# Optimization experiments

Hardware: AMD Instinct MI355X
Metric: run time of the kernel (lower is better)

## Reference

```python
import jax, jax.numpy as jnp
import numpy as np

B, T, D, H = 2, 2048, 1024, 16
DK = D // H
NEG = -1e9  # stand-in for -inf; causal mask guarantees >=1 valid key per row


def setup_inputs() -> dict:
    key = jax.random.key(0)
    ks = jax.random.split(key, 9)
    s = 1.0 / np.sqrt(D)
    x = jax.random.normal(ks[0], (B, T, D), dtype=jnp.float32)
    mask = jnp.broadcast_to(jnp.tril(jnp.ones((T, T), dtype=jnp.int32))[None, None], (B, 1, T, T))
    params = {}
    for i, n in enumerate(['q', 'k', 'v', 'o']):
        params['W' + n] = jax.random.normal(ks[1 + 2 * i], (D, D), dtype=jnp.float32) * s
        params['b' + n] = jax.random.normal(ks[2 + 2 * i], (D,), dtype=jnp.float32) * s
    return dict(x=x, mask=mask, **params)


def reference(x, mask, Wq, bq, Wk, bk, Wv, bv, Wo, bo):
    Bx, Tx, Dx = x.shape
    # projections: [B,T,D] -> [B,H,T,DK]
    def split_heads(y):
        return y.reshape(Bx, Tx, H, DK).transpose(0, 2, 1, 3)
    Q = split_heads(x @ Wq + bq)
    K = split_heads(x @ Wk + bk)
    V = split_heads(x @ Wv + bv)
    scores = jnp.einsum('bhqd,bhkd->bhqk', Q, K) / jnp.sqrt(jnp.float32(DK))
    scores = jnp.where(mask == 0, NEG, scores)
    attn = jax.nn.softmax(scores, axis=-1)  # dropout is identity in eval / p=0
    out = jnp.einsum('bhqk,bhkd->bhqd', attn, V)
    out = out.transpose(0, 2, 1, 3).reshape(Bx, Tx, Dx)
    return out @ Wo + bo
```

## Files before the change

kernel.cpp:

```cpp
#include <hip/hip_runtime.h>
#include <hip/hip_bf16.h>

typedef __bf16 bf16;
typedef __attribute__((ext_vector_type(8))) __bf16 bf16x8;
typedef __attribute__((ext_vector_type(4))) __bf16 bf16x4;
typedef __attribute__((ext_vector_type(4))) float f32x4;

#define TSEQ 2048
#define DMODEL 1024
#define NHEAD 16
#define DKH 64
#define BATCH 2
#define NQKV 3072
#define PSTR 72

typedef __attribute__((address_space(1))) const void gv_t;
typedef __attribute__((address_space(3))) void sv_t;
__device__ __forceinline__ void gll16(const bf16* g, bf16* s) {
    __builtin_amdgcn_global_load_lds((gv_t*)g, (sv_t*)s, 16, 0, 0);
}
__device__ __forceinline__ void wait_vm0() {
    __builtin_amdgcn_s_waitcnt(0x0F70);
}

__global__ __launch_bounds__(256) void prologue(
    const float* __restrict__ x,
    const float* __restrict__ W0, const float* __restrict__ W1,
    const float* __restrict__ W2, const float* __restrict__ W3,
    const float* __restrict__ bq, const float* __restrict__ bk,
    const float* __restrict__ bv,
    bf16* __restrict__ xb, bf16* __restrict__ WT, float* __restrict__ wsBias)
{
    __shared__ float t[32][33];
    const int bid = blockIdx.x, tid = threadIdx.x;
    if (bid < 4096) {
        const int mz = bid >> 10, tt = bid & 1023;
        const float* W = mz == 0 ? W0 : mz == 1 ? W1 : mz == 2 ? W2 : W3;
        bf16* T = WT + (size_t)mz * DMODEL * DMODEL;
        const int bx = (tt & 31) * 32, by = (tt >> 5) * 32;
        const int tx = tid & 31, ty = tid >> 5;
#pragma unroll
        for (int i = 0; i < 4; ++i)
            t[ty + i * 8][tx] = W[(size_t)(by + ty + i * 8) * DMODEL + bx + tx];
        __syncthreads();
#pragma unroll
        for (int i = 0; i < 4; ++i)
            T[(size_t)(bx + ty + i * 8) * DMODEL + by + tx] = (bf16)t[tx][ty + i * 8];
    } else if (bid < 8192) {
        int i = ((bid - 4096) * 256 + tid) * 4;
        f32x4 v = *(const f32x4*)(x + i);
        bf16x4 o;
#pragma unroll
        for (int j = 0; j < 4; ++j) o[j] = (bf16)v[j];
        *(bf16x4*)(xb + i) = o;
    } else {
        int i = (bid - 8192) * 256 + tid;
        wsBias[i] = i < 1024 ? bq[i] : i < 2048 ? bk[i - 1024] : bv[i - 2048];
    }
}

template <typename OutT>
__global__ __launch_bounds__(256) void gemm_bias_kernel(
    const bf16* __restrict__ A, const bf16* __restrict__ BT,
    const float* __restrict__ bias, OutT* __restrict__ C0,
    OutT* __restrict__ C1, int ldc, bf16* __restrict__ Vout, int ksteps)
{
    __shared__ bf16 As[128 * 32];
    __shared__ bf16 Bs[128 * 32];
    const int tid = threadIdx.x;
    const int ln = tid & 63, wave = tid >> 6;
    const int wm = wave >> 1, wn = wave & 1;
    const int lr = ln & 15, quad = ln >> 4;
    const int m0 = blockIdx.y * 128, n0 = blockIdx.x * 128;
    const int k0 = blockIdx.z * ksteps * 32;
    OutT* C = blockIdx.z == 0 ? C0 : C1;

    f32x4 acc[4][4] = {};

    const int grow = wave * 32 + (ln >> 2);
    const int gch = (ln & 3) ^ ((ln >> 2) & 3);
    const bf16* Ag = A + (size_t)(m0 + grow) * DMODEL + gch * 8;
    const bf16* Bg = BT + (size_t)(n0 + grow) * DMODEL + gch * 8;
    bf16* AsW = As + wave * 1024;
    bf16* BsW = Bs + wave * 1024;
    const int rsw = (lr & 3);

    for (int kt = 0; kt < ksteps; ++kt) {
        const int kk = k0 + kt * 32;
        gll16(Ag + kk, AsW);
        gll16(Ag + (size_t)16 * DMODEL + kk, AsW + 512);
        gll16(Bg + kk, BsW);
        gll16(Bg + (size_t)16 * DMODEL + kk, BsW + 512);
        wait_vm0();
        __syncthreads();
        bf16x8 af[4], bfr[4];
#pragma unroll
        for (int i = 0; i < 4; ++i)
            af[i] = *(const bf16x8*)(As + (wm * 64 + i * 16 + lr) * 32 +
                                     ((quad ^ rsw) * 8));
#pragma unroll
        for (int j = 0; j < 4; ++j)
            bfr[j] = *(const bf16x8*)(Bs + (wn * 64 + j * 16 + lr) * 32 +
                                      ((quad ^ rsw) * 8));
#pragma unroll
        for (int i = 0; i < 4; ++i)
#pragma unroll
            for (int j = 0; j < 4; ++j)
                acc[i][j] = __builtin_amdgcn_mfma_f32_16x16x32_bf16(
                    af[i], bfr[j], acc[i][j], 0, 0, 0);
        __syncthreads();
    }

    if (Vout != nullptr && n0 >= 2048) {
        const int bb = m0 >> 11;
        const int tb_ = (m0 & (TSEQ - 1)) + wm * 64;
#pragma unroll
        for (int j = 0; j < 4; ++j) {
            int n = n0 + wn * 64 + j * 16 + lr;
            int hd = n - 2048;
            float bv = bias[n];
            bf16* vrow = Vout + ((size_t)(bb * DMODEL + hd)) * TSEQ;
#pragma unroll
            for (int i = 0; i < 4; ++i) {
                int t = tb_ + i * 16 + quad * 4;
                bf16x4 v4;
#pragma unroll
                for (int r = 0; r < 4; ++r) v4[r] = (bf16)(acc[i][j][r] + bv);
                *(bf16x4*)(vrow + t) = v4;
            }
        }
    } else {
#pragma unroll
        for (int j = 0; j < 4; ++j) {
            int n = n0 + wn * 64 + j * 16 + lr;
            float bv = bias ? bias[n] : 0.f;
#pragma unroll
            for (int i = 0; i < 4; ++i) {
                int mb = m0 + wm * 64 + i * 16 + quad * 4;
#pragma unroll
                for (int r = 0; r < 4; ++r)
                    C[(size_t)(mb + r) * ldc + n] = (OutT)(acc[i][j][r] + bv);
            }
        }
    }
}

__global__ __launch_bounds__(256) void reduce_out(
    const float* __restrict__ P1, const float* __restrict__ bias,
    float* __restrict__ out)
{
    int i = (blockIdx.x * 256 + threadIdx.x) * 4;
    f32x4 a = *(const f32x4*)(out + i);
    f32x4 b = *(const f32x4*)(P1 + i);
    f32x4 bi = *(const f32x4*)(bias + (i & (DMODEL - 1)));
    f32x4 r = a + b + bi;
    *(f32x4*)(out + i) = r;
}

template <bool MASK>
__device__ __forceinline__ void attn_chunk(
    int kc, int q0w, int lr, int quad,
    const bf16* __restrict__ KsB, const bf16* __restrict__ VsB,
    bf16* __restrict__ Pw,
    const bf16x8 qb[2], f32x4 oacc[4], float& lrow)
{
    const int sw = lr & 7;
    bf16x8 kb[4][2];
#pragma unroll
    for (int kt = 0; kt < 4; ++kt)
#pragma unroll
        for (int kk = 0; kk < 2; ++kk)
            kb[kt][kk] = *(const bf16x8*)(KsB + (kt * 16 + lr) * 64 +
                                          (((kk * 4 + quad) ^ sw) * 8));
    f32x4 st[4] = {};
#pragma unroll
    for (int kt = 0; kt < 4; ++kt)
#pragma unroll
        for (int kk = 0; kk < 2; ++kk)
            st[kt] = __builtin_amdgcn_mfma_f32_16x16x32_bf16(
                kb[kt][kk], qb[kk], st[kt], 0, 0, 0);

    const float scale2 = 0.18033688f;
    const int q = q0w + lr;
    float rs = 0.f;
#pragma unroll
    for (int kt = 0; kt < 4; ++kt) {
        bf16x4 p4;
#pragma unroll
        for (int r = 0; r < 4; ++r) {
            float p = exp2f(fmaf(st[kt][r], scale2, -24.0f));
            if (MASK && (kc + kt * 16 + quad * 4 + r > q)) p = 0.f;
            rs += p;
            p4[r] = (bf16)p;
        }
        *(bf16x4*)(Pw + lr * PSTR + kt * 16 + quad * 4) = p4;
    }
    rs += __shfl_xor(rs, 16);
    rs += __shfl_xor(rs, 32);
    lrow += rs;

#pragma unroll
    for (int kk = 0; kk < 2; ++kk) {
        bf16x8 pa = *(const bf16x8*)(Pw + lr * PSTR + kk * 32 + quad * 8);
#pragma unroll
        for (int dt = 0; dt < 4; ++dt) {
            bf16x8 vb = *(const bf16x8*)(VsB + (dt * 16 + lr) * 64 +
                                         (((kk * 4 + quad) ^ sw) * 8));
            oacc[dt] = __builtin_amdgcn_mfma_f32_16x16x32_bf16(
                pa, vb, oacc[dt], 0, 0, 0);
        }
    }
}

__global__ __launch_bounds__(512) void flash_attn(
    const bf16* __restrict__ QKV, const bf16* __restrict__ VT,
    bf16* __restrict__ O)
{
    __shared__ bf16 Ks[2][64 * 64];
    __shared__ bf16 Vs[2][64 * 64];
    __shared__ bf16 Pl[8][16 * PSTR];
    const int tid = threadIdx.x;
    const int ln = tid & 63, w = tid >> 6;
    const int lr = ln & 15, quad = ln >> 4;
    const int h = blockIdx.y, b = blockIdx.z;

    int xb = blockIdx.x;
    if ((h ^ b) & 1) xb = (TSEQ / 128 - 1) - xb;
    const int q0 = xb * 128;
    const int q0w = q0 + w * 16;
    bf16* Pw = Pl[w];

    const bf16* Qb = QKV + (size_t)b * TSEQ * NQKV + h * DKH;
    const bf16* Kb = Qb + 1024;
    const bf16* VTb = VT + (size_t)(b * NHEAD + h) * DKH * TSEQ;

    const int srow = (w & 3) * 16 + (ln >> 3);
    const int scol = ((ln & 7) ^ ((ln >> 3) & 7)) * 8;
    const bool stK = (w < 4);

    auto stage = [&](int buf, int kc) {
        if (stK) {
            const bf16* g = Kb + (size_t)(kc + srow) * NQKV + scol;
            bf16* s = &Ks[buf][(w & 3) * 16 * 64];
#pragma unroll
            for (int l = 0; l < 2; ++l)
                gll16(g + (size_t)(l * 8) * NQKV, s + l * 8 * 64);
        } else {
            const bf16* g = VTb + (size_t)srow * TSEQ + kc + scol;
            bf16* s = &Vs[buf][(w & 3) * 16 * 64];
#pragma unroll
            for (int l = 0; l < 2; ++l)
                gll16(g + (size_t)(l * 8) * TSEQ, s + l * 8 * 64);
        }
    };

    bf16x8 qb[2];
#pragma unroll
    for (int kk = 0; kk < 2; ++kk)
        qb[kk] = *(const bf16x8*)(Qb + (size_t)(q0w + lr) * NQKV +
                                  kk * 32 + quad * 8);

    f32x4 oacc[4] = {};
    float lrow = 0.f;

    const int nch = (q0 + 128) >> 6;
    stage(0, 0);
    wait_vm0();
    __syncthreads();
    for (int c = 0; c < nch; ++c) {
        if (c + 1 < nch) stage((c + 1) & 1, (c + 1) * 64);
        const int kc = c * 64;
        if (kc <= q0w + 15) {
            if (kc + 63 <= q0w)
                attn_chunk<false>(kc, q0w, lr, quad, Ks[c & 1], Vs[c & 1], Pw,
                                  qb, oacc, lrow);
            else
                attn_chunk<true>(kc, q0w, lr, quad, Ks[c & 1], Vs[c & 1], Pw,
                                 qb, oacc, lrow);
        }
        wait_vm0();
        __syncthreads();
    }

#pragma unroll
    for (int r = 0; r < 4; ++r) {
        float inv = 1.0f / __shfl(lrow, quad * 4 + r);
        int row = q0w + quad * 4 + r;
#pragma unroll
        for (int dt = 0; dt < 4; ++dt)
            O[(size_t)(b * TSEQ + row) * DMODEL + h * DKH + dt * 16 + lr] =
                (bf16)(oacc[dt][r] * inv);
    }
}

extern "C" void kernel_launch(void* const* d_in, const int* in_sizes, int n_in,
                              void* d_out, int out_size, void* d_ws, size_t ws_size,
                              hipStream_t stream)
{
    const float* x  = (const float*)d_in[0];
    const float* Wq = (const float*)d_in[2];
    const float* bq = (const float*)d_in[3];
    const float* Wk = (const float*)d_in[4];
    const float* bk = (const float*)d_in[5];
    const float* Wv = (const float*)d_in[6];
    const float* bv = (const float*)d_in[7];
    const float* Wo = (const float*)d_in[8];
    const float* bo = (const float*)d_in[9];

    char* ws = (char*)d_ws;
    bf16* xb   = (bf16*)(ws);
    bf16* QKV  = (bf16*)(ws + (8u  << 20));
    bf16* VT   = (bf16*)(ws + (32u << 20));
    bf16* O    = (bf16*)(ws + (40u << 20));
    bf16* WT   = (bf16*)(ws + (48u << 20));
    float* wsBias = (float*)O;
    float* P1  = (float*)QKV;

    prologue<<<8204, 256, 0, stream>>>(x, Wq, Wk, Wv, Wo, bq, bk, bv,
                                       xb, WT, wsBias);

    gemm_bias_kernel<bf16><<<dim3(NQKV / 128, 32, 1), 256, 0, stream>>>(
        xb, WT, wsBias, QKV, QKV, NQKV, VT, DMODEL / 32);

    flash_attn<<<dim3(TSEQ / 128, NHEAD, BATCH), 512, 0, stream>>>(QKV, VT, O);

    gemm_bias_kernel<float><<<dim3(DMODEL / 128, 32, 2), 256, 0, stream>>>(
        O, WT + 3u * (1u << 20), nullptr, (float*)d_out, P1, DMODEL, nullptr,
        DMODEL / 64);

    reduce_out<<<(BATCH * TSEQ * DMODEL) / 1024, 256, 0, stream>>>(
        P1, bo, (float*)d_out);
}
```

Measured before the change: 232.9 us.

## Multi-stage async LDS pipeline in GEMM and drop split-K output reduction

The GEMM kernel now uses a 4-buffer LDS ring fed by global_load_lds. Three k-steps are prefetched ahead, and partial vmcnt waits replace a full drain plus two barriers per step. The output projection no longer uses a 2-way split-K, so the separate reduce_out kernel and its fp32 partial buffer are removed and the bias is added in the GEMM epilogue. The LDS XOR swizzle is also dropped, which may add bank conflicts. The 64KB of shared memory reduces occupancy, and the output GEMM now runs only 256 blocks.

```diff
diff --git a/kernel.cpp b/kernel.cpp
--- a/kernel.cpp
+++ b/kernel.cpp
@@ -19,8 +19,9 @@
 __device__ __forceinline__ void gll16(const bf16* g, bf16* s) {
     __builtin_amdgcn_global_load_lds((gv_t*)g, (sv_t*)s, 16, 0, 0);
 }
-__device__ __forceinline__ void wait_vm0() {
-    __builtin_amdgcn_s_waitcnt(0x0F70);
+template <int N>
+__device__ __forceinline__ void wait_vm() {
+    __builtin_amdgcn_s_waitcnt(0x0F70 | N);
 }
 
 __global__ __launch_bounds__(256) void prologue(
@@ -62,54 +63,61 @@
 template <typename OutT>
 __global__ __launch_bounds__(256) void gemm_bias_kernel(
     const bf16* __restrict__ A, const bf16* __restrict__ BT,
-    const float* __restrict__ bias, OutT* __restrict__ C0,
-    OutT* __restrict__ C1, int ldc, bf16* __restrict__ Vout, int ksteps)
-{
-    __shared__ bf16 As[128 * 32];
-    __shared__ bf16 Bs[128 * 32];
+    const float* __restrict__ bias, OutT* __restrict__ C, int ldc,
+    bf16* __restrict__ Vout)
+{
+    __shared__ bf16 As[4][128 * 32];
+    __shared__ bf16 Bs[4][128 * 32];
     const int tid = threadIdx.x;
     const int ln = tid & 63, wave = tid >> 6;
     const int wm = wave >> 1, wn = wave & 1;
     const int lr = ln & 15, quad = ln >> 4;
     const int m0 = blockIdx.y * 128, n0 = blockIdx.x * 128;
-    const int k0 = blockIdx.z * ksteps * 32;
-    OutT* C = blockIdx.z == 0 ? C0 : C1;
 
     f32x4 acc[4][4] = {};
 
     const int grow = wave * 32 + (ln >> 2);
-    const int gch = (ln & 3) ^ ((ln >> 2) & 3);
-    const bf16* Ag = A + (size_t)(m0 + grow) * DMODEL + gch * 8;
-    const bf16* Bg = BT + (size_t)(n0 + grow) * DMODEL + gch * 8;
-    bf16* AsW = As + wave * 1024;
-    bf16* BsW = Bs + wave * 1024;
-    const int rsw = (lr & 3);
-
-    for (int kt = 0; kt < ksteps; ++kt) {
-        const int kk = k0 + kt * 32;
-        gll16(Ag + kk, AsW);
-        gll16(Ag + (size_t)16 * DMODEL + kk, AsW + 512);
-        gll16(Bg + kk, BsW);
-        gll16(Bg + (size_t)16 * DMODEL + kk, BsW + 512);
-        wait_vm0();
-        __syncthreads();
+    const int gcol = (ln & 3) * 8;
+    const bf16* Ag = A + (size_t)(m0 + grow) * DMODEL + gcol;
+    const bf16* Bg = BT + (size_t)(n0 + grow) * DMODEL + gcol;
+
+    auto stage = [&](int buf, int kt) {
+        const int kk = kt * 32;
+        bf16* aw = &As[buf][wave * 1024];
+        bf16* bw = &Bs[buf][wave * 1024];
+        gll16(Ag + kk, aw);
+        gll16(Ag + (size_t)16 * DMODEL + kk, aw + 512);
+        gll16(Bg + kk, bw);
+        gll16(Bg + (size_t)16 * DMODEL + kk, bw + 512);
+    };
+
+    auto compute = [&](int buf) {
         bf16x8 af[4], bfr[4];
 #pragma unroll
         for (int i = 0; i < 4; ++i)
-            af[i] = *(const bf16x8*)(As + (wm * 64 + i * 16 + lr) * 32 +
-                                     ((quad ^ rsw) * 8));
+            af[i] = *(const bf16x8*)(&As[buf][(wm * 64 + i * 16 + lr) * 32 + quad * 8]);
 #pragma unroll
         for (int j = 0; j < 4; ++j)
-            bfr[j] = *(const bf16x8*)(Bs + (wn * 64 + j * 16 + lr) * 32 +
-                                      ((quad ^ rsw) * 8));
+            bfr[j] = *(const bf16x8*)(&Bs[buf][(wn * 64 + j * 16 + lr) * 32 + quad * 8]);
 #pragma unroll
         for (int i = 0; i < 4; ++i)
 #pragma unroll
             for (int j = 0; j < 4; ++j)
                 acc[i][j] = __builtin_amdgcn_mfma_f32_16x16x32_bf16(
                     af[i], bfr[j], acc[i][j], 0, 0, 0);
+    };
+
+    stage(0, 0); stage(1, 1); stage(2, 2);
+
+    for (int k = 0; k < 29; ++k) {
+        wait_vm<8>();
         __syncthreads();
-    }
+        stage((k + 3) & 3, k + 3);
+        compute(k & 3);
+    }
+    wait_vm<8>(); __syncthreads(); compute(1);
+    wait_vm<4>(); __syncthreads(); compute(2);
+    wait_vm<0>(); __syncthreads(); compute(3);
 
     if (Vout != nullptr && n0 >= 2048) {
         const int bb = m0 >> 11;
@@ -133,7 +141,7 @@
 #pragma unroll
         for (int j = 0; j < 4; ++j) {
             int n = n0 + wn * 64 + j * 16 + lr;
-            float bv = bias ? bias[n] : 0.f;
+            float bv = bias[n];
 #pragma unroll
             for (int i = 0; i < 4; ++i) {
                 int mb = m0 + wm * 64 + i * 16 + quad * 4;
@@ -143,18 +151,6 @@
             }
         }
     }
-}
-
-__global__ __launch_bounds__(256) void reduce_out(
-    const float* __restrict__ P1, const float* __restrict__ bias,
-    float* __restrict__ out)
-{
-    int i = (blockIdx.x * 256 + threadIdx.x) * 4;
-    f32x4 a = *(const f32x4*)(out + i);
-    f32x4 b = *(const f32x4*)(P1 + i);
-    f32x4 bi = *(const f32x4*)(bias + (i & (DMODEL - 1)));
-    f32x4 r = a + b + bi;
-    *(f32x4*)(out + i) = r;
 }
 
 template <bool MASK>
@@ -265,7 +261,7 @@
 
     const int nch = (q0 + 128) >> 6;
     stage(0, 0);
-    wait_vm0();
+    wait_vm<0>();
     __syncthreads();
     for (int c = 0; c < nch; ++c) {
         if (c + 1 < nch) stage((c + 1) & 1, (c + 1) * 64);
@@ -278,7 +274,7 @@
                 attn_chunk<true>(kc, q0w, lr, quad, Ks[c & 1], Vs[c & 1], Pw,
                                  qb, oacc, lrow);
         }
-        wait_vm0();
+        wait_vm<0>();
         __syncthreads();
     }
 
@@ -314,20 +310,15 @@
     bf16* O    = (bf16*)(ws + (40u << 20));
     bf16* WT   = (bf16*)(ws + (48u << 20));
     float* wsBias = (float*)O;
-    float* P1  = (float*)QKV;
 
     prologue<<<8204, 256, 0, stream>>>(x, Wq, Wk, Wv, Wo, bq, bk, bv,
                                        xb, WT, wsBias);
 
-    gemm_bias_kernel<bf16><<<dim3(NQKV / 128, 32, 1), 256, 0, stream>>>(
-        xb, WT, wsBias, QKV, QKV, NQKV, VT, DMODEL / 32);
+    gemm_bias_kernel<bf16><<<dim3(NQKV / 128, 32), 256, 0, stream>>>(
+        xb, WT, wsBias, QKV, NQKV, VT);
 
     flash_attn<<<dim3(TSEQ / 128, NHEAD, BATCH), 512, 0, stream>>>(QKV, VT, O);
 
-    gemm_bias_kernel<float><<<dim3(DMODEL / 128, 32, 2), 256, 0, stream>>>(
-        O, WT + 3u * (1u << 20), nullptr, (float*)d_out, P1, DMODEL, nullptr,
-        DMODEL / 64);
-
-    reduce_out<<<(BATCH * TSEQ * DMODEL) / 1024, 256, 0, stream>>>(
-        P1, bo, (float*)d_out);
-}
+    gemm_bias_kernel<float><<<dim3(DMODEL / 128, 32), 256, 0, stream>>>(
+        O, WT + 3u * (1u << 20), bo, (float*)d_out, DMODEL, nullptr);
+}
```

Result: no change. 232.3 us (-0.3%).
